# Kernel optimization log

Measured on AMD Instinct MI355X. Metric: run time of the kernel, lower is better.

The kernel has to match this reference:

```python
import jax, jax.numpy as jnp
import numpy as np
import math

D = 2048
NH = 16
HD = D // NH
MULT = 4
EPS = 1e-6


def rmsnorm(x, g):
    norm = jax.lax.rsqrt(jnp.mean(x * x, axis=-1, keepdims=True) + EPS)
    return g * x * norm


def setup_inputs() -> dict:
    key = jax.random.key(0)
    ks = jax.random.split(key, 8)
    s = 0.02  # keep activations in a sane range
    return {
        "x": jax.random.normal(ks[0], (2, 2048, D), dtype=jnp.float32),
        "g1": jnp.ones((D,), dtype=jnp.float32),
        "wq": jax.random.normal(ks[1], (D, D), dtype=jnp.float32) * s,
        "wk": jax.random.normal(ks[2], (D, D), dtype=jnp.float32) * s,
        "wv": jax.random.normal(ks[3], (D, D), dtype=jnp.float32) * s,
        "wo": jax.random.normal(ks[4], (D, D), dtype=jnp.float32) * s,
        "g2": jnp.ones((D,), dtype=jnp.float32),
        "w_up": jax.random.normal(ks[5], (2 * D * MULT, D), dtype=jnp.float32) * s,
        "w_down": jax.random.normal(ks[6], (D, D * MULT), dtype=jnp.float32) * s,
    }


def reference(x, g1, wq, wk, wv, wo, g2, w_up, w_down):
    B, T, _ = x.shape
    # --- causal self-attention with pre-RMSNorm ---
    h = rmsnorm(x, g1)
    q = (h @ wq.T).reshape(B, T, NH, HD).transpose(0, 2, 1, 3)  # [B,H,T,hd]
    k = (h @ wk.T).reshape(B, T, NH, HD).transpose(0, 2, 1, 3)
    v = (h @ wv.T).reshape(B, T, NH, HD).transpose(0, 2, 1, 3)
    att = jnp.einsum("bhtd,bhsd->bhts", q, k) / math.sqrt(HD)  # [B,H,T,T]
    neg = jnp.finfo(att.dtype).min
    causal = jnp.triu(jnp.full((T, T), neg, dtype=att.dtype), k=1)
    att = att + causal
    w = jax.nn.softmax(att, axis=-1)
    z = jnp.einsum("bhts,bhsd->bhtd", w, v)  # [B,H,T,hd]
    z = z.transpose(0, 2, 1, 3).reshape(B, T, D)
    x = x + z @ wo.T
    # --- SwiGLU-style FFN (GELU gate) with pre-RMSNorm ---
    h2 = rmsnorm(x, g2)
    uv = h2 @ w_up.T  # [B,T,2*D*MULT]
    u, vgate = jnp.split(uv, 2, axis=-1)
    ff = (jax.nn.gelu(u, approximate=False) * vgate) @ w_down.T
    return x + ff
```

## Files before the change

### kernel.cpp

```cpp
#include <hip/hip_runtime.h>
#include <math.h>

typedef __bf16 bf16_t;
typedef __bf16 bf16x8 __attribute__((ext_vector_type(8)));
typedef __bf16 bf16x4 __attribute__((ext_vector_type(4)));
typedef float f32x4 __attribute__((ext_vector_type(4)));

#define D_MODEL 2048
#define N_HEADS 16
#define HEAD_D 128
#define SEQ 2048
#define NTOK 4096
#define DFF 8192
#define UPN 16384

#define GLDS16(g, l) __builtin_amdgcn_global_load_lds( \
    (const __attribute__((address_space(1))) void*)(g), \
    (__attribute__((address_space(3))) void*)(l), 16, 0, 0)

#define MFMA16(a, b, c) __builtin_amdgcn_mfma_f32_16x16x32_bf16((a), (b), (c), 0, 0, 0)

__global__ __launch_bounds__(256) void cvt_bf16_kernel(const float* __restrict__ in,
                                                       bf16_t* __restrict__ out, long n4) {
    long i = (long)blockIdx.x * 256 + threadIdx.x;
    long stride = (long)gridDim.x * 256;
    for (; i < n4; i += stride) {
        float4 f = ((const float4*)in)[i];
        bf16x4 v;
        v[0] = (bf16_t)f.x; v[1] = (bf16_t)f.y; v[2] = (bf16_t)f.z; v[3] = (bf16_t)f.w;
        ((bf16x4*)out)[i] = v;
    }
}

__global__ __launch_bounds__(256) void rmsnorm_kernel(const float* __restrict__ x,
                                                      const float* __restrict__ g,
                                                      bf16_t* __restrict__ out) {
    int row = blockIdx.x;
    const float* xr = x + (size_t)row * D_MODEL;
    int c0 = threadIdx.x * 8;
    float4 a = *(const float4*)&xr[c0];
    float4 b = *(const float4*)&xr[c0 + 4];
    float ss = a.x*a.x + a.y*a.y + a.z*a.z + a.w*a.w
             + b.x*b.x + b.y*b.y + b.z*b.z + b.w*b.w;
    #pragma unroll
    for (int off = 1; off < 64; off <<= 1) ss += __shfl_xor(ss, off);
    __shared__ float red[4];
    if ((threadIdx.x & 63) == 0) red[threadIdx.x >> 6] = ss;
    __syncthreads();
    float norm = rsqrtf((red[0] + red[1] + red[2] + red[3]) * (1.f / D_MODEL) + 1e-6f);
    float4 ga = *(const float4*)&g[c0];
    float4 gb = *(const float4*)&g[c0 + 4];
    bf16x8 o;
    o[0] = (bf16_t)(a.x * ga.x * norm); o[1] = (bf16_t)(a.y * ga.y * norm);
    o[2] = (bf16_t)(a.z * ga.z * norm); o[3] = (bf16_t)(a.w * ga.w * norm);
    o[4] = (bf16_t)(b.x * gb.x * norm); o[5] = (bf16_t)(b.y * gb.y * norm);
    o[6] = (bf16_t)(b.z * gb.z * norm); o[7] = (bf16_t)(b.w * gb.w * norm);
    *(bf16x8*)&out[(size_t)row * D_MODEL + c0] = o;
}

__global__ __launch_bounds__(256) void combine3_kernel(const float* __restrict__ r,
        const float* __restrict__ p0, const float* __restrict__ p1,
        float* __restrict__ out, long n4) {
    long i = (long)blockIdx.x * 256 + threadIdx.x;
    long stride = (long)gridDim.x * 256;
    for (; i < n4; i += stride) {
        float4 a = ((const float4*)r)[i];
        float4 b = ((const float4*)p0)[i];
        float4 c = ((const float4*)p1)[i];
        float4 o; o.x = a.x+b.x+c.x; o.y = a.y+b.y+c.y; o.z = a.z+b.z+c.z; o.w = a.w+b.w+c.w;
        ((float4*)out)[i] = o;
    }
}

template<int MODE, int KSPLIT>
__global__ __launch_bounds__(512, 2)
void gemm256(const bf16_t* __restrict__ A, const bf16_t* __restrict__ W,
             void* __restrict__ o0, void* __restrict__ o1, void* __restrict__ o2,
             const float* __restrict__ res, int nbx, int K)
{
    __shared__ __align__(16) bf16_t ldsA[2 * 2 * 8192];
    __shared__ __align__(16) bf16_t ldsB[2 * 2 * 8192];
    const int tid = threadIdx.x;
    const int wave = tid >> 6, lane = tid & 63;
    const int lr = lane & 15, lg = lane >> 4;
    const int wm = wave >> 2, wn = wave & 3;

    const int nwg = gridDim.x, bid = blockIdx.x;
    const int cpx = nwg >> 3;
    const int s = (bid & 7) * cpx + (bid >> 3);
    const int by = s & 15, bx = s >> 4;
    const int bm0 = by * 256;
    const int bn0 = (MODE == 2) ? bx * 128 : bx * 256;
    const int z = (KSPLIT == 2) ? blockIdx.z : 0;
    const int Keff = K / KSPLIT, koff = z * Keff;

    const int rl = wave * 16 + (lane >> 2);
    const int gsw = ((lane & 3) ^ ((rl >> 1) & 3)) * 8;
    const bf16_t* asrc = A + (size_t)(bm0 + rl) * K + koff + gsw;
    const bf16_t* bsrc;
    size_t bstep2;
    if constexpr (MODE == 2) {
        int grp = rl >> 6, wi = rl & 63;
        int brow = (wi < 32) ? (bn0 + grp * 32 + wi) : (DFF + bn0 + grp * 32 + (wi - 32));
        bsrc = W + (size_t)brow * K + koff + gsw;
        bstep2 = (size_t)64 * K;
    } else {
        bsrc = W + (size_t)(bn0 + rl) * K + koff + gsw;
        bstep2 = (size_t)128 * K;
    }

    auto stA = [&](int t, int kh) {
        char* d = (char*)ldsA + (((t & 1) * 2 + kh) * 16384) + wave * 1024 + lane * 16;
        const bf16_t* sp = asrc + (size_t)t * 64 + kh * 32;
        GLDS16(sp, d);
        GLDS16(sp + (size_t)128 * K, d + 8192);
    };
    auto stB = [&](int t, int kh) {
        char* d = (char*)ldsB + (((t & 1) * 2 + kh) * 16384) + wave * 1024 + lane * 16;
        const bf16_t* sp = bsrc + (size_t)t * 64 + kh * 32;
        GLDS16(sp, d);
        GLDS16(sp + bstep2, d + 8192);
    };

    f32x4 acc[8][4] = {};
    const int xg = (lg ^ ((lr >> 1) & 3)) * 8;
    const int NKT = Keff >> 6;

    stA(0, 0); stA(0, 1); stB(0, 0); stB(0, 1); stA(1, 0);
    asm volatile("s_waitcnt vmcnt(2)" ::: "memory");
    __builtin_amdgcn_s_barrier();

    for (int t = 0; t < NKT; ++t) {
        const bf16_t* Ab = ldsA + ((t & 1) * 2) * 8192;
        const bf16_t* Bb = ldsB + ((t & 1) * 2) * 8192;
        const bool s1 = (t + 1 < NKT), s2 = (t + 2 < NKT);
        bf16x8 a0[4], a1[4], b0[4], b1[4];

        #pragma unroll
        for (int i = 0; i < 4; ++i)
            a0[i] = *(const bf16x8*)&Ab[(wm * 128 + i * 16 + lr) * 32 + xg];
        #pragma unroll
        for (int n = 0; n < 4; ++n)
            b0[n] = *(const bf16x8*)&Bb[(wn * 64 + n * 16 + lr) * 32 + xg];
        if (s1) { stA(t + 1, 1); stB(t + 1, 0); }
        __builtin_amdgcn_s_setprio(1);
        #pragma unroll
        for (int i = 0; i < 4; ++i)
            #pragma unroll
            for (int n = 0; n < 4; ++n)
                acc[i][n] = MFMA16(a0[i], b0[n], acc[i][n]);
        __builtin_amdgcn_s_setprio(0);

        #pragma unroll
        for (int i = 0; i < 4; ++i)
            a1[i] = *(const bf16x8*)&Ab[(wm * 128 + (i + 4) * 16 + lr) * 32 + xg];
        if (s1) stB(t + 1, 1);
        __builtin_amdgcn_s_setprio(1);
        #pragma unroll
        for (int i = 0; i < 4; ++i)
            #pragma unroll
            for (int n = 0; n < 4; ++n)
                acc[i + 4][n] = MFMA16(a1[i], b0[n], acc[i + 4][n]);
        __builtin_amdgcn_s_setprio(0);
        __builtin_amdgcn_s_barrier();

        #pragma unroll
        for (int i = 0; i < 4; ++i)
            a0[i] = *(const bf16x8*)&Ab[8192 + (wm * 128 + i * 16 + lr) * 32 + xg];
        #pragma unroll
        for (int n = 0; n < 4; ++n)
            b1[n] = *(const bf16x8*)&Bb[8192 + (wn * 64 + n * 16 + lr) * 32 + xg];
        __builtin_amdgcn_s_setprio(1);
        #pragma unroll
        for (int i = 0; i < 4; ++i)
            #pragma unroll
            for (int n = 0; n < 4; ++n)
                acc[i][n] = MFMA16(a0[i], b1[n], acc[i][n]);
        __builtin_amdgcn_s_setprio(0);

        #pragma unroll
        for (int i = 0; i < 4; ++i)
            a1[i] = *(const bf16x8*)&Ab[8192 + (wm * 128 + (i + 4) * 16 + lr) * 32 + xg];
        if (s2) stA(t + 2, 0);
        __builtin_amdgcn_s_setprio(1);
        #pragma unroll
        for (int i = 0; i < 4; ++i)
            #pragma unroll
            for (int n = 0; n < 4; ++n)
                acc[i + 4][n] = MFMA16(a1[i], b1[n], acc[i + 4][n]);
        __builtin_amdgcn_s_setprio(0);
        if (s2) asm volatile("s_waitcnt vmcnt(2)" ::: "memory");
        else    asm volatile("s_waitcnt vmcnt(0)" ::: "memory");
        __builtin_amdgcn_s_barrier();
    }

    if constexpr (MODE == 0) {
        const float qs = 0.08838834764831845f;
        const int th = bn0 >> 11;
        #pragma unroll
        for (int m = 0; m < 8; ++m) {
            int grow = bm0 + wm * 128 + m * 16 + lg * 4;
            #pragma unroll
            for (int n = 0; n < 4; ++n) {
                int gcol = bn0 + wn * 64 + n * 16 + lr;
                int c = gcol & 2047;
                if (th == 0) {
                    #pragma unroll
                    for (int r = 0; r < 4; ++r)
                        ((bf16_t*)o0)[(size_t)(grow + r) * D_MODEL + c] = (bf16_t)(acc[m][n][r] * qs);
                } else if (th == 1) {
                    #pragma unroll
                    for (int r = 0; r < 4; ++r)
                        ((bf16_t*)o1)[(size_t)(grow + r) * D_MODEL + c] = (bf16_t)acc[m][n][r];
                } else {
                    int hh = c >> 7, d = c & 127;
                    int bb = grow >> 11, t0 = grow & 2047;
                    bf16x4 st;
                    #pragma unroll
                    for (int r = 0; r < 4; ++r) st[r] = (bf16_t)acc[m][n][r];
                    *(bf16x4*)&((bf16_t*)o2)[((size_t)(bb * N_HEADS + hh) * HEAD_D + d) * SEQ + t0] = st;
                }
            }
        }
    } else if constexpr (MODE == 1) {
        float* po = (KSPLIT == 2) ? ((float*)o0 + (size_t)z * NTOK * D_MODEL) : (float*)o0;
        #pragma unroll
        for (int m = 0; m < 8; ++m) {
            int grow = bm0 + wm * 128 + m * 16 + lg * 4;
            #pragma unroll
            for (int n = 0; n < 4; ++n) {
                int gcol = bn0 + wn * 64 + n * 16 + lr;
                #pragma unroll
                for (int r = 0; r < 4; ++r) {
                    size_t idx = (size_t)(grow + r) * D_MODEL + gcol;
                    if (KSPLIT == 2) po[idx] = acc[m][n][r];
                    else             po[idx] = res[idx] + acc[m][n][r];
                }
            }
        }
    } else {
        #pragma unroll
        for (int m = 0; m < 8; ++m) {
            int grow = bm0 + wm * 128 + m * 16 + lg * 4;
            #pragma unroll
            for (int n = 0; n < 2; ++n) {
                int gcol = bn0 + wn * 32 + n * 16 + lr;
                #pragma unroll
                for (int r = 0; r < 4; ++r) {
                    float u = acc[m][n][r], vg = acc[m][n + 2][r];
                    float ge = 0.5f * u * (1.f + erff(u * 0.70710678118654752f));
                    ((bf16_t*)o0)[(size_t)(grow + r) * DFF + gcol] = (bf16_t)(ge * vg);
                }
            }
        }
    }
}

__global__ __launch_bounds__(256)
void attn_kernel(const bf16_t* __restrict__ Q, const bf16_t* __restrict__ K,
                 const bf16_t* __restrict__ Vt, bf16_t* __restrict__ Z)
{
    const int qt = gridDim.x - 1 - blockIdx.x;
    const int h = blockIdx.y, b = blockIdx.z;
    const int q0 = qt * 64;
    const int tid = threadIdx.x, wave = tid >> 6, lane = tid & 63;
    const int lr = lane & 15, lg = lane >> 4;

    __shared__ __align__(16) bf16_t Qs[64 * 136];
    __shared__ __align__(16) bf16_t Ks[64 * 136];
    __shared__ __align__(16) bf16_t Vts[128 * 72];
    __shared__ __align__(16) bf16_t Ps[4][16 * 72];

    const size_t base = ((size_t)b * SEQ) * D_MODEL + (size_t)h * HEAD_D;
    const size_t vbase = (size_t)(b * N_HEADS + h) * HEAD_D * SEQ;

    #pragma unroll
    for (int i = 0; i < 4; ++i) {
        int v = tid + 256 * i;
        int row = v >> 4, cv = (v & 15) * 8;
        *(uint4*)&Qs[row * 136 + cv] = *(const uint4*)&Q[base + (size_t)(q0 + row) * D_MODEL + cv];
    }

    f32x4 o[8] = {};
    float mrun[4], lrun[4];
    #pragma unroll
    for (int r = 0; r < 4; ++r) { mrun[r] = -1e30f; lrun[r] = 0.f; }

    for (int kt = 0; kt <= qt; ++kt) {
        const int k0 = kt * 64;
        __syncthreads();
        #pragma unroll
        for (int i = 0; i < 4; ++i) {
            int v = tid + 256 * i;
            int row = v >> 4, cv = (v & 15) * 8;
            *(uint4*)&Ks[row * 136 + cv] = *(const uint4*)&K[base + (size_t)(k0 + row) * D_MODEL + cv];
            int d = v >> 3, c8 = (v & 7) * 8;
            *(uint4*)&Vts[d * 72 + c8] = *(const uint4*)&Vt[vbase + (size_t)d * SEQ + k0 + c8];
        }
        __syncthreads();

        f32x4 sv[4] = {};
        #pragma unroll
        for (int kk = 0; kk < 4; ++kk) {
            bf16x8 aq = *(const bf16x8*)&Qs[(wave * 16 + lr) * 136 + kk * 32 + lg * 8];
            #pragma unroll
            for (int nb = 0; nb < 4; ++nb) {
                bf16x8 bk = *(const bf16x8*)&Ks[(nb * 16 + lr) * 136 + kk * 32 + lg * 8];
                sv[nb] = MFMA16(aq, bk, sv[nb]);
            }
        }
        if (kt == qt) {
            #pragma unroll
            for (int nb = 0; nb < 4; ++nb)
                #pragma unroll
                for (int r = 0; r < 4; ++r) {
                    int qrel = 16 * wave + lg * 4 + r;
                    int krel = nb * 16 + lr;
                    if (krel > qrel) sv[nb][r] = -1e30f;
                }
        }
        float resc[4];
        #pragma unroll
        for (int r = 0; r < 4; ++r) {
            float mx = fmaxf(fmaxf(sv[0][r], sv[1][r]), fmaxf(sv[2][r], sv[3][r]));
            #pragma unroll
            for (int off = 1; off < 16; off <<= 1) mx = fmaxf(mx, __shfl_xor(mx, off));
            float mnew = fmaxf(mrun[r], mx);
            resc[r] = __expf(mrun[r] - mnew);
            float sum = 0.f;
            #pragma unroll
            for (int nb = 0; nb < 4; ++nb) {
                float p = __expf(sv[nb][r] - mnew);
                sv[nb][r] = p;
                sum += p;
            }
            #pragma unroll
            for (int off = 1; off < 16; off <<= 1) sum += __shfl_xor(sum, off);
            lrun[r] = lrun[r] * resc[r] + sum;
            mrun[r] = mnew;
        }
        #pragma unroll
        for (int ob = 0; ob < 8; ++ob)
            #pragma unroll
            for (int r = 0; r < 4; ++r) o[ob][r] *= resc[r];
        #pragma unroll
        for (int nb = 0; nb < 4; ++nb)
            #pragma unroll
            for (int r = 0; r < 4; ++r)
                Ps[wave][(lg * 4 + r) * 72 + nb * 16 + lr] = (bf16_t)sv[nb][r];
        #pragma unroll
        for (int kk = 0; kk < 2; ++kk) {
            bf16x8 ap = *(const bf16x8*)&Ps[wave][lr * 72 + kk * 32 + lg * 8];
            #pragma unroll
            for (int ob = 0; ob < 8; ++ob) {
                bf16x8 bv = *(const bf16x8*)&Vts[(ob * 16 + lr) * 72 + kk * 32 + lg * 8];
                o[ob] = MFMA16(ap, bv, o[ob]);
            }
        }
    }
    #pragma unroll
    for (int ob = 0; ob < 8; ++ob)
        #pragma unroll
        for (int r = 0; r < 4; ++r) {
            int t = q0 + 16 * wave + lg * 4 + r;
            Z[base + (size_t)t * D_MODEL + ob * 16 + lr] = (bf16_t)(o[ob][r] / lrun[r]);
        }
}

extern "C" void kernel_launch(void* const* d_in, const int* in_sizes, int n_in,
                              void* d_out, int out_size, void* d_ws, size_t ws_size,
                              hipStream_t stream)
{
    const float* x   = (const float*)d_in[0];
    const float* g1  = (const float*)d_in[1];
    const float* wq  = (const float*)d_in[2];
    const float* wk  = (const float*)d_in[3];
    const float* wv  = (const float*)d_in[4];
    const float* wo  = (const float*)d_in[5];
    const float* g2  = (const float*)d_in[6];
    const float* wup = (const float*)d_in[7];
    const float* wdn = (const float*)d_in[8];
    float* out = (float*)d_out;

    char* wsp = (char*)d_ws;
    size_t off = 0;
    auto alloc = [&](size_t bytes) { void* p = wsp + off; off += (bytes + 255) & ~255ull; return p; };
    bf16_t* wq_b  = (bf16_t*)alloc((size_t)D_MODEL * D_MODEL * 2);
    bf16_t* wk_b  = (bf16_t*)alloc((size_t)D_MODEL * D_MODEL * 2);
    bf16_t* wv_b  = (bf16_t*)alloc((size_t)D_MODEL * D_MODEL * 2);
    bf16_t* wo_b  = (bf16_t*)alloc((size_t)D_MODEL * D_MODEL * 2);
    bf16_t* wup_b = (bf16_t*)alloc((size_t)UPN * D_MODEL * 2);
    bf16_t* wdn_b = (bf16_t*)alloc((size_t)D_MODEL * DFF * 2);
    bf16_t* h_b   = (bf16_t*)alloc((size_t)NTOK * D_MODEL * 2);
    bf16_t* q_b   = (bf16_t*)alloc((size_t)NTOK * D_MODEL * 2);
    bf16_t* k_b   = (bf16_t*)alloc((size_t)NTOK * D_MODEL * 2);
    bf16_t* vt_b  = (bf16_t*)alloc((size_t)NTOK * D_MODEL * 2);
    bf16_t* z_b   = (bf16_t*)alloc((size_t)NTOK * D_MODEL * 2);
    float*  x1    = (float*) alloc((size_t)NTOK * D_MODEL * 4);
    bf16_t* h2_b  = (bf16_t*)alloc((size_t)NTOK * D_MODEL * 2);
    bf16_t* act_b = (bf16_t*)alloc((size_t)NTOK * DFF * 2);
    float* pbuf = (float*)h_b;

    auto cvt = [&](const float* in, bf16_t* outb, long n) {
        long n4 = n / 4;
        long nb = (n4 + 255) / 256;
        int blocks = nb > 2048 ? 2048 : (int)nb;
        cvt_bf16_kernel<<<blocks, 256, 0, stream>>>(in, outb, n4);
    };
    cvt(wq,  wq_b,  (long)D_MODEL * D_MODEL);
    cvt(wk,  wk_b,  (long)D_MODEL * D_MODEL);
    cvt(wv,  wv_b,  (long)D_MODEL * D_MODEL);
    cvt(wo,  wo_b,  (long)D_MODEL * D_MODEL);
    cvt(wup, wup_b, (long)UPN * D_MODEL);
    cvt(wdn, wdn_b, (long)D_MODEL * DFF);

    rmsnorm_kernel<<<NTOK, 256, 0, stream>>>(x, g1, h_b);

    gemm256<0, 1><<<24 * 16, 512, 0, stream>>>(h_b, wq_b, q_b, k_b, vt_b, nullptr, 24, D_MODEL);

    attn_kernel<<<dim3(SEQ / 64, N_HEADS, 2), 256, 0, stream>>>(q_b, k_b, vt_b, z_b);

    gemm256<1, 2><<<dim3(8 * 16, 1, 2), 512, 0, stream>>>(z_b, wo_b, pbuf, nullptr, nullptr, nullptr, 8, D_MODEL);
    combine3_kernel<<<2048, 256, 0, stream>>>(x, pbuf, pbuf + (size_t)NTOK * D_MODEL, x1,
                                              (long)NTOK * D_MODEL / 4);

    rmsnorm_kernel<<<NTOK, 256, 0, stream>>>(x1, g2, h2_b);

    gemm256<2, 1><<<64 * 16, 512, 0, stream>>>(h2_b, wup_b, act_b, nullptr, nullptr, nullptr, 64, D_MODEL);

    gemm256<1, 2><<<dim3(8 * 16, 1, 2), 512, 0, stream>>>(act_b, wdn_b, pbuf, nullptr, nullptr, nullptr, 8, DFF);
    combine3_kernel<<<2048, 256, 0, stream>>>(x1, pbuf, pbuf + (size_t)NTOK * D_MODEL, out,
                                              (long)NTOK * D_MODEL / 4);
}
```

Measured before the change: 1.006 ms.

## Deepen GEMM prefetch pipeline with symmetric A/B staging and peeled tail iterations

Changes the K-loop software pipeline so both the A and B half-tiles for step t+1 are issued a stage earlier, and loads for t+2 are interleaved symmetrically. More global-to-LDS loads stay in flight across the compute phases, using finer vmcnt(8) waits instead of draining to vmcnt(2). The last two iterations are peeled via a macro with constant wait counts, which removes runtime branches on the tail. The risk is miscounted vmcnt values producing LDS races, and more code size from the macro expansion.

Measured after the change: 968.3 us. 1.04x faster.

```diff
diff --git a/kernel.cpp b/kernel.cpp
--- a/kernel.cpp
+++ b/kernel.cpp
@@ -126,73 +126,80 @@
     const int xg = (lg ^ ((lr >> 1) & 3)) * 8;
     const int NKT = Keff >> 6;
 
-    stA(0, 0); stA(0, 1); stB(0, 0); stB(0, 1); stA(1, 0);
-    asm volatile("s_waitcnt vmcnt(2)" ::: "memory");
+    stA(0, 0); stB(0, 0); stA(0, 1); stB(0, 1); stA(1, 0); stB(1, 0);
+    asm volatile("s_waitcnt vmcnt(8)" ::: "memory");
     __builtin_amdgcn_s_barrier();
 
-    for (int t = 0; t < NKT; ++t) {
-        const bf16_t* Ab = ldsA + ((t & 1) * 2) * 8192;
-        const bf16_t* Bb = ldsB + ((t & 1) * 2) * 8192;
-        const bool s1 = (t + 1 < NKT), s2 = (t + 2 < NKT);
-        bf16x8 a0[4], a1[4], b0[4], b1[4];
-
-        #pragma unroll
-        for (int i = 0; i < 4; ++i)
-            a0[i] = *(const bf16x8*)&Ab[(wm * 128 + i * 16 + lr) * 32 + xg];
-        #pragma unroll
-        for (int n = 0; n < 4; ++n)
-            b0[n] = *(const bf16x8*)&Bb[(wn * 64 + n * 16 + lr) * 32 + xg];
-        if (s1) { stA(t + 1, 1); stB(t + 1, 0); }
-        __builtin_amdgcn_s_setprio(1);
-        #pragma unroll
-        for (int i = 0; i < 4; ++i)
-            #pragma unroll
-            for (int n = 0; n < 4; ++n)
-                acc[i][n] = MFMA16(a0[i], b0[n], acc[i][n]);
-        __builtin_amdgcn_s_setprio(0);
-
-        #pragma unroll
-        for (int i = 0; i < 4; ++i)
-            a1[i] = *(const bf16x8*)&Ab[(wm * 128 + (i + 4) * 16 + lr) * 32 + xg];
-        if (s1) stB(t + 1, 1);
-        __builtin_amdgcn_s_setprio(1);
-        #pragma unroll
-        for (int i = 0; i < 4; ++i)
-            #pragma unroll
-            for (int n = 0; n < 4; ++n)
-                acc[i + 4][n] = MFMA16(a1[i], b0[n], acc[i + 4][n]);
-        __builtin_amdgcn_s_setprio(0);
-        __builtin_amdgcn_s_barrier();
-
-        #pragma unroll
-        for (int i = 0; i < 4; ++i)
-            a0[i] = *(const bf16x8*)&Ab[8192 + (wm * 128 + i * 16 + lr) * 32 + xg];
-        #pragma unroll
-        for (int n = 0; n < 4; ++n)
-            b1[n] = *(const bf16x8*)&Bb[8192 + (wn * 64 + n * 16 + lr) * 32 + xg];
-        __builtin_amdgcn_s_setprio(1);
-        #pragma unroll
-        for (int i = 0; i < 4; ++i)
-            #pragma unroll
-            for (int n = 0; n < 4; ++n)
-                acc[i][n] = MFMA16(a0[i], b1[n], acc[i][n]);
-        __builtin_amdgcn_s_setprio(0);
-
-        #pragma unroll
-        for (int i = 0; i < 4; ++i)
-            a1[i] = *(const bf16x8*)&Ab[8192 + (wm * 128 + (i + 4) * 16 + lr) * 32 + xg];
-        if (s2) stA(t + 2, 0);
-        __builtin_amdgcn_s_setprio(1);
-        #pragma unroll
-        for (int i = 0; i < 4; ++i)
-            #pragma unroll
-            for (int n = 0; n < 4; ++n)
-                acc[i + 4][n] = MFMA16(a1[i], b1[n], acc[i + 4][n]);
-        __builtin_amdgcn_s_setprio(0);
-        if (s2) asm volatile("s_waitcnt vmcnt(2)" ::: "memory");
-        else    asm volatile("s_waitcnt vmcnt(0)" ::: "memory");
-        __builtin_amdgcn_s_barrier();
-    }
+#define TILE_BODY(T, S1, S2, W1, W2)                                                    \
+    {                                                                                   \
+        const int t_ = (T);                                                             \
+        const bf16_t* Ab = ldsA + ((t_ & 1) * 2) * 8192;                                \
+        const bf16_t* Bb = ldsB + ((t_ & 1) * 2) * 8192;                                \
+        bf16x8 a0[4], a1[4], b0[4], b1[4];                                              \
+                                                                      \
+        _Pragma("unroll")                                                               \
+        for (int i = 0; i < 4; ++i)                                                     \
+            a0[i] = *(const bf16x8*)&Ab[(wm * 128 + i * 16 + lr) * 32 + xg];            \
+        _Pragma("unroll")                                                               \
+        for (int n = 0; n < 4; ++n)                                                     \
+            b0[n] = *(const bf16x8*)&Bb[(wn * 64 + n * 16 + lr) * 32 + xg];             \
+        if (S1) stA(t_ + 1, 1);                                                         \
+        __builtin_amdgcn_s_setprio(1);                                                  \
+        _Pragma("unroll")                                                               \
+        for (int i = 0; i < 4; ++i)                                                     \
+            _Pragma("unroll")                                                           \
+            for (int n = 0; n < 4; ++n)                                                 \
+                acc[i][n] = MFMA16(a0[i], b0[n], acc[i][n]);                            \
+        __builtin_amdgcn_s_setprio(0);                                                  \
+                                                                      \
+        _Pragma("unroll")                                                               \
+        for (int i = 0; i < 4; ++i)                                                     \
+            a1[i] = *(const bf16x8*)&Ab[(wm * 128 + (i + 4) * 16 + lr) * 32 + xg];      \
+        if (S1) stB(t_ + 1, 1);                                                         \
+        __builtin_amdgcn_s_setprio(1);                                                  \
+        _Pragma("unroll")                                                               \
+        for (int i = 0; i < 4; ++i)                                                     \
+            _Pragma("unroll")                                                           \
+            for (int n = 0; n < 4; ++n)                                                 \
+                acc[i + 4][n] = MFMA16(a1[i], b0[n], acc[i + 4][n]);                    \
+        __builtin_amdgcn_s_setprio(0);                                                  \
+        asm volatile("s_waitcnt vmcnt(" W1 ")" ::: "memory");                           \
+        __builtin_amdgcn_s_barrier();                                                   \
+                                                                      \
+        _Pragma("unroll")                                                               \
+        for (int i = 0; i < 4; ++i)                                                     \
+            a0[i] = *(const bf16x8*)&Ab[8192 + (wm * 128 + i * 16 + lr) * 32 + xg];     \
+        _Pragma("unroll")                                                               \
+        for (int n = 0; n < 4; ++n)                                                     \
+            b1[n] = *(const bf16x8*)&Bb[8192 + (wn * 64 + n * 16 + lr) * 32 + xg];      \
+        if (S2) stA(t_ + 2, 0);                                                         \
+        __builtin_amdgcn_s_setprio(1);                                                  \
+        _Pragma("unroll")                                                               \
+        for (int i = 0; i < 4; ++i)                                                     \
+            _Pragma("unroll")                                                           \
+            for (int n = 0; n < 4; ++n)                                                 \
+                acc[i][n] = MFMA16(a0[i], b1[n], acc[i][n]);                            \
+        __builtin_amdgcn_s_setprio(0);                                                  \
+                                                                      \
+        _Pragma("unroll")                                                               \
+        for (int i = 0; i < 4; ++i)                                                     \
+            a1[i] = *(const bf16x8*)&Ab[8192 + (wm * 128 + (i + 4) * 16 + lr) * 32 + xg]; \
+        if (S2) stB(t_ + 2, 0);                                                         \
+        __builtin_amdgcn_s_setprio(1);                                                  \
+        _Pragma("unroll")                                                               \
+        for (int i = 0; i < 4; ++i)                                                     \
+            _Pragma("unroll")                                                           \
+            for (int n = 0; n < 4; ++n)                                                 \
+                acc[i + 4][n] = MFMA16(a1[i], b1[n], acc[i + 4][n]);                    \
+        __builtin_amdgcn_s_setprio(0);                                                  \
+        asm volatile("s_waitcnt vmcnt(" W2 ")" ::: "memory");                           \
+        __builtin_amdgcn_s_barrier();                                                   \
+    }
+
+    for (int t = 0; t < NKT - 2; ++t) TILE_BODY(t, true, true, "8", "8");
+    TILE_BODY(NKT - 2, true, false, "8", "4");
+    TILE_BODY(NKT - 1, false, false, "0", "0");
+#undef TILE_BODY
 
     if constexpr (MODE == 0) {
         const float qs = 0.08838834764831845f;
```
